# Kernel tuning notes

Hardware: AMD Instinct MI355X
Metric: run time of the kernel (lower is better)

The kernel has to match this reference:

```python
import jax, jax.numpy as jnp
import numpy as np
import math

DIM = 768
FFN_DIM = 4 * DIM
EPS = 1e-5

def layer_norm(x, gamma, beta):
    mu = jnp.mean(x, axis=-1, keepdims=True)
    var = jnp.var(x, axis=-1, keepdims=True)
    return (x - mu) * jax.lax.rsqrt(var + EPS) * gamma + beta

def setup_inputs() -> dict:
    key = jax.random.key(0)
    ks = jax.random.split(key, 8)
    b, n, d = 8, 2048, DIM
    s = 1.0 / math.sqrt(d)
    x = jax.random.normal(ks[0], (b, n, d), dtype=jnp.float32)
    Wq = jax.random.normal(ks[1], (d, d), dtype=jnp.float32) * s
    Wk = jax.random.normal(ks[2], (d, d), dtype=jnp.float32) * s
    Wv = jax.random.normal(ks[3], (d, d), dtype=jnp.float32) * s
    W1 = jax.random.normal(ks[4], (d, FFN_DIM), dtype=jnp.float32) * s
    b1 = jnp.zeros((FFN_DIM,), dtype=jnp.float32)
    W2 = jax.random.normal(ks[5], (FFN_DIM, d), dtype=jnp.float32) * (1.0 / math.sqrt(FFN_DIM))
    b2 = jnp.zeros((d,), dtype=jnp.float32)
    g1 = jnp.ones((d,), dtype=jnp.float32); be1 = jnp.zeros((d,), dtype=jnp.float32)
    g2 = jnp.ones((d,), dtype=jnp.float32); be2 = jnp.zeros((d,), dtype=jnp.float32)
    return {"x": x, "Wq": Wq, "Wk": Wk, "Wv": Wv, "ln1_g": g1, "ln1_b": be1,
            "W1": W1, "b1": b1, "W2": W2, "b2": b2, "ln2_g": g2, "ln2_b": be2}

def reference(x, Wq, Wk, Wv, ln1_g, ln1_b, W1, b1, W2, b2, ln2_g, ln2_b):
    # Self-attention (single head, full dim; dropout in eval mode => identity)
    Q = jnp.einsum('bnd,de->bne', x, Wq)
    K = jnp.einsum('bnd,de->bne', x, Wk)
    V = jnp.einsum('bnd,de->bne', x, Wv)
    scores = jnp.einsum('bnd,bmd->bnm', Q, K) / math.sqrt(DIM)  # [b,n,n]
    attn = jax.nn.softmax(scores, axis=-1)
    O = jnp.einsum('bnm,bmd->bnd', attn, V)
    h = layer_norm(x + O, ln1_g, ln1_b)
    # FFN with exact GELU (torch nn.GELU default)
    hidden = jax.nn.gelu(jnp.einsum('bnd,df->bnf', h, W1) + b1, approximate=False)
    out = jnp.einsum('bnf,fd->bnd', hidden, W2) + b2
    return layer_norm(h + out, ln2_g, ln2_b)
```

## Files before the change

### kernel.cpp

```cpp
#include <hip/hip_runtime.h>
#include <hip/hip_bf16.h>
#include <math.h>

using u16 = unsigned short;
typedef __bf16 bf16x8 __attribute__((ext_vector_type(8)));
typedef float f32x4 __attribute__((ext_vector_type(4)));
typedef u16 u16x8 __attribute__((ext_vector_type(8)));

__device__ __forceinline__ u16 f2b(float f) {
  union { float f; unsigned u; } c; c.f = f;
  unsigned r = c.u + 0x7fffu + ((c.u >> 16) & 1u);
  return (u16)(r >> 16);
}
__device__ __forceinline__ float b2f(u16 h) {
  union { unsigned u; float f; } c; c.u = ((unsigned)h) << 16;
  return c.f;
}

#define EPI_BF16 0
#define EPI_BF16_SCALE 1
#define EPI_GELU_BIAS 2
#define EPI_F32_BIAS 3

#define GLDS16(src, dst)                                                     \
  __builtin_amdgcn_global_load_lds(                                          \
      (const __attribute__((address_space(1))) void*)(src),                  \
      (__attribute__((address_space(3))) void*)(dst), 16, 0, 0)

__device__ __forceinline__ int xswz(int o, int n) {
  int q = n >> 3, r = n & 7, x = o & 7, i = o >> 3;
  return (x < r ? x * (q + 1) : r * (q + 1) + (x - r) * q) + i;
}

template <int EPI>
__global__ __launch_bounds__(512, 2) void gemm256(
    const u16* __restrict__ Ag, const u16* __restrict__ Bg,
    void* __restrict__ Cg, const float* __restrict__ bias,
    int nbx, int K, float scale, int lda, int ldb, int ldc,
    long long sAz, long long sBz, long long sCz)
{
  __shared__ __align__(16) u16 lds[65536];

  const int tid = threadIdx.x;
  const int wave = tid >> 6, lane = tid & 63;
  const int wr = wave >> 2, wc = wave & 3;
  const int id = xswz(blockIdx.x, gridDim.x);
  const int bx = id % nbx, by = id / nbx;
  const int m0 = by * 256, n0 = bx * 256;
  const long long z = blockIdx.z;
  const u16* A = Ag + z * sAz + (long long)m0 * lda;
  const u16* B = Bg + z * sBz + (long long)n0 * ldb;

  const int rA = wave * 32 + (lane >> 2);
  const int slot = (lane & 3) ^ ((rA >> 1) & 3);
  const u16* a0 = A + (long long)rA * lda + slot * 8;
  const u16* a1 = a0 + (long long)16 * lda;
  const u16* b0 = B + (long long)rA * ldb + slot * 8;
  const u16* b1 = b0 + (long long)16 * ldb;
  const int d0 = wave * 32 * 32;
  const int d1 = (wave * 32 + 16) * 32;

  int offA[8], offB[4];
#pragma unroll
  for (int mf = 0; mf < 8; ++mf) {
    int r = wr * 128 + mf * 16 + (lane & 15);
    int b = r * 64 + ((lane >> 4) << 4);
    offA[mf] = b ^ (((b >> 7) & 3) << 4);
  }
#pragma unroll
  for (int nf = 0; nf < 4; ++nf) {
    int r = wc * 64 + nf * 16 + (lane & 15);
    int b = r * 64 + ((lane >> 4) << 4);
    offB[nf] = b ^ (((b >> 7) & 3) << 4);
  }

  f32x4 acc[8][4];
#pragma unroll
  for (int m = 0; m < 8; ++m)
#pragma unroll
    for (int n = 0; n < 4; ++n) acc[m][n] = f32x4{0.f, 0.f, 0.f, 0.f};

  const char* ldsc = (const char*)lds;
  const int NT = K >> 6;

  GLDS16(a0, lds + 0 * 8192 + d0);  GLDS16(a1, lds + 0 * 8192 + d1);
  GLDS16(b0, lds + 2 * 8192 + d0);  GLDS16(b1, lds + 2 * 8192 + d1);
  GLDS16(a0 + 32, lds + 1 * 8192 + d0);  GLDS16(a1 + 32, lds + 1 * 8192 + d1);
  GLDS16(b0 + 32, lds + 3 * 8192 + d0);  GLDS16(b1 + 32, lds + 3 * 8192 + d1);
  asm volatile("s_waitcnt vmcnt(4)" ::: "memory");
  asm volatile("s_barrier" ::: "memory");

  for (int t = 0; t < NT; ++t) {
    const int buf = t & 1, nb = buf ^ 1;
    const int kc = (t + 1 < NT) ? ((t + 1) << 6) : 0;
    const char* pA0 = ldsc + (buf * 4 + 0) * 16384;
    const char* pA1 = ldsc + (buf * 4 + 1) * 16384;
    const char* pB0 = ldsc + (buf * 4 + 2) * 16384;
    const char* pB1 = ldsc + (buf * 4 + 3) * 16384;
    u16* q = lds + nb * 4 * 8192;

    bf16x8 Af[4], Bf[4];

    GLDS16(a0 + kc, q + 0 * 8192 + d0);
    GLDS16(a1 + kc, q + 0 * 8192 + d1);
#pragma unroll
    for (int m = 0; m < 4; ++m) Af[m] = *(const bf16x8*)(pA0 + offA[m]);
#pragma unroll
    for (int n = 0; n < 4; ++n) Bf[n] = *(const bf16x8*)(pB0 + offB[n]);
    asm volatile("s_barrier" ::: "memory");
    __builtin_amdgcn_s_setprio(1);
#pragma unroll
    for (int m = 0; m < 4; ++m)
#pragma unroll
      for (int n = 0; n < 4; ++n)
        acc[m][n] = __builtin_amdgcn_mfma_f32_16x16x32_bf16(Af[m], Bf[n], acc[m][n], 0, 0, 0);
    __builtin_amdgcn_s_setprio(0);
    asm volatile("s_barrier" ::: "memory");

    GLDS16(b0 + kc, q + 2 * 8192 + d0);
    GLDS16(b1 + kc, q + 2 * 8192 + d1);
#pragma unroll
    for (int m = 0; m < 4; ++m) Af[m] = *(const bf16x8*)(pA0 + offA[4 + m]);
    asm volatile("s_barrier" ::: "memory");
    __builtin_amdgcn_s_setprio(1);
#pragma unroll
    for (int m = 0; m < 4; ++m)
#pragma unroll
      for (int n = 0; n < 4; ++n)
        acc[4 + m][n] = __builtin_amdgcn_mfma_f32_16x16x32_bf16(Af[m], Bf[n], acc[4 + m][n], 0, 0, 0);
    __builtin_amdgcn_s_setprio(0);
    asm volatile("s_waitcnt vmcnt(4)" ::: "memory");
    asm volatile("s_barrier" ::: "memory");

    GLDS16(a0 + kc + 32, q + 1 * 8192 + d0);
    GLDS16(a1 + kc + 32, q + 1 * 8192 + d1);
#pragma unroll
    for (int m = 0; m < 4; ++m) Af[m] = *(const bf16x8*)(pA1 + offA[m]);
#pragma unroll
    for (int n = 0; n < 4; ++n) Bf[n] = *(const bf16x8*)(pB1 + offB[n]);
    asm volatile("s_barrier" ::: "memory");
    __builtin_amdgcn_s_setprio(1);
#pragma unroll
    for (int m = 0; m < 4; ++m)
#pragma unroll
      for (int n = 0; n < 4; ++n)
        acc[m][n] = __builtin_amdgcn_mfma_f32_16x16x32_bf16(Af[m], Bf[n], acc[m][n], 0, 0, 0);
    __builtin_amdgcn_s_setprio(0);
    asm volatile("s_barrier" ::: "memory");

    GLDS16(b0 + kc + 32, q + 3 * 8192 + d0);
    GLDS16(b1 + kc + 32, q + 3 * 8192 + d1);
#pragma unroll
    for (int m = 0; m < 4; ++m) Af[m] = *(const bf16x8*)(pA1 + offA[4 + m]);
    asm volatile("s_barrier" ::: "memory");
    __builtin_amdgcn_s_setprio(1);
#pragma unroll
    for (int m = 0; m < 4; ++m)
#pragma unroll
      for (int n = 0; n < 4; ++n)
        acc[4 + m][n] = __builtin_amdgcn_mfma_f32_16x16x32_bf16(Af[m], Bf[n], acc[4 + m][n], 0, 0, 0);
    __builtin_amdgcn_s_setprio(0);
    asm volatile("s_waitcnt vmcnt(4)" ::: "memory");
    asm volatile("s_barrier" ::: "memory");
  }

#pragma unroll
  for (int mf = 0; mf < 8; ++mf) {
#pragma unroll
    for (int nf = 0; nf < 4; ++nf) {
      const int crow = m0 + wr * 128 + mf * 16 + (lane >> 4) * 4;
      const int ccol = n0 + wc * 64 + nf * 16 + (lane & 15);
#pragma unroll
      for (int j = 0; j < 4; ++j) {
        const float v = acc[mf][nf][j];
        const long long off = (long long)(crow + j) * ldc + ccol + z * sCz;
        if (EPI == EPI_BF16) {
          ((u16*)Cg)[off] = f2b(v);
        } else if (EPI == EPI_BF16_SCALE) {
          ((u16*)Cg)[off] = f2b(v * scale);
        } else if (EPI == EPI_GELU_BIAS) {
          const float t2 = v + bias[ccol];
          const float g = 0.5f * t2 * (1.0f + erff(t2 * 0.70710678118654752440f));
          ((u16*)Cg)[off] = f2b(g);
        } else {
          ((float*)Cg)[off] = v + bias[ccol];
        }
      }
    }
  }
}

__global__ __launch_bounds__(256) void cast_f32_bf16(
    const float* __restrict__ x, u16* __restrict__ y, long long n4)
{
  const long long i = (long long)blockIdx.x * 256 + threadIdx.x;
  if (i >= n4) return;
  const float4 v = ((const float4*)x)[i];
  ushort4 o;
  o.x = f2b(v.x); o.y = f2b(v.y); o.z = f2b(v.z); o.w = f2b(v.w);
  ((ushort4*)y)[i] = o;
}

template <bool SRC_BF16>
__global__ __launch_bounds__(256) void transpose_cast(
    const void* __restrict__ srcv, u16* __restrict__ dst, int R, int C, int ldsrc,
    long long szSrc, long long szDst)
{
  __shared__ float tile[32][33];
  const long long zs = (long long)blockIdx.z * szSrc;
  const long long zd = (long long)blockIdx.z * szDst;
  const int c0 = blockIdx.x * 32, r0 = blockIdx.y * 32;
  const int tx = threadIdx.x & 31, ty = threadIdx.x >> 5;
#pragma unroll
  for (int i = 0; i < 4; ++i) {
    const int r = r0 + ty + i * 8;
    float v;
    if (SRC_BF16) v = b2f(((const u16*)srcv)[zs + (long long)r * ldsrc + c0 + tx]);
    else          v = ((const float*)srcv)[zs + (long long)r * ldsrc + c0 + tx];
    tile[ty + i * 8][tx] = v;
  }
  __syncthreads();
#pragma unroll
  for (int i = 0; i < 4; ++i) {
    const int c = c0 + ty + i * 8;
    dst[zd + (long long)c * R + r0 + tx] = f2b(tile[tx][ty + i * 8]);
  }
}

__global__ __launch_bounds__(256) void softmax_rows(
    u16* __restrict__ S, int ncol)
{
  __shared__ float red[8];
  const long long row = blockIdx.x;
  u16* s = S + row * ncol;
  const int t = threadIdx.x;

  const u16x8 u = *(const u16x8*)&s[t * 8];
  float v[8];
#pragma unroll
  for (int j = 0; j < 8; ++j) v[j] = b2f(u[j]);

  float mx = v[0];
#pragma unroll
  for (int j = 1; j < 8; ++j) mx = fmaxf(mx, v[j]);
  for (int o = 32; o; o >>= 1) mx = fmaxf(mx, __shfl_xor(mx, o));
  if ((t & 63) == 0) red[t >> 6] = mx;
  __syncthreads();
  mx = fmaxf(fmaxf(red[0], red[1]), fmaxf(red[2], red[3]));

  float sum = 0.f;
#pragma unroll
  for (int j = 0; j < 8; ++j) { v[j] = __expf(v[j] - mx); sum += v[j]; }
  for (int o = 32; o; o >>= 1) sum += __shfl_xor(sum, o);
  if ((t & 63) == 0) red[4 + (t >> 6)] = sum;
  __syncthreads();
  sum = red[4] + red[5] + red[6] + red[7];

  const float inv = 1.0f / sum;
  u16x8 o8;
#pragma unroll
  for (int j = 0; j < 8; ++j) o8[j] = f2b(v[j] * inv);
  *(u16x8*)&s[t * 8] = o8;
}

__global__ __launch_bounds__(256) void ln1_kernel(
    const float* __restrict__ x, const u16* __restrict__ O,
    const float* __restrict__ g, const float* __restrict__ be,
    u16* __restrict__ h)
{
  __shared__ float red[8];
  const long long row = blockIdx.x;
  const float* xr = x + row * 768;
  const u16* orow = O + row * 768;
  const int t = threadIdx.x, base = t * 3;

  float v[3];
#pragma unroll
  for (int j = 0; j < 3; ++j) v[j] = xr[base + j] + b2f(orow[base + j]);
  float s = v[0] + v[1] + v[2];
  float ss = v[0] * v[0] + v[1] * v[1] + v[2] * v[2];
  for (int o = 32; o; o >>= 1) { s += __shfl_xor(s, o); ss += __shfl_xor(ss, o); }
  if ((t & 63) == 0) { red[t >> 6] = s; red[4 + (t >> 6)] = ss; }
  __syncthreads();
  s = red[0] + red[1] + red[2] + red[3];
  ss = red[4] + red[5] + red[6] + red[7];
  const float mu = s * (1.0f / 768.0f);
  const float var = ss * (1.0f / 768.0f) - mu * mu;
  const float inv = rsqrtf(var + 1e-5f);
#pragma unroll
  for (int j = 0; j < 3; ++j) {
    const float o = (v[j] - mu) * inv * g[base + j] + be[base + j];
    h[row * 768 + base + j] = f2b(o);
  }
}

__global__ __launch_bounds__(256) void ln2_kernel(
    const u16* __restrict__ h, const float* __restrict__ oflt,
    const float* __restrict__ g, const float* __restrict__ be,
    float* __restrict__ y)
{
  __shared__ float red[8];
  const long long row = blockIdx.x;
  const u16* hr = h + row * 768;
  const float* orow = oflt + row * 768;
  const int t = threadIdx.x, base = t * 3;

  float v[3];
#pragma unroll
  for (int j = 0; j < 3; ++j) v[j] = b2f(hr[base + j]) + orow[base + j];
  float s = v[0] + v[1] + v[2];
  float ss = v[0] * v[0] + v[1] * v[1] + v[2] * v[2];
  for (int o = 32; o; o >>= 1) { s += __shfl_xor(s, o); ss += __shfl_xor(ss, o); }
  if ((t & 63) == 0) { red[t >> 6] = s; red[4 + (t >> 6)] = ss; }
  __syncthreads();
  s = red[0] + red[1] + red[2] + red[3];
  ss = red[4] + red[5] + red[6] + red[7];
  const float mu = s * (1.0f / 768.0f);
  const float var = ss * (1.0f / 768.0f) - mu * mu;
  const float inv = rsqrtf(var + 1e-5f);
#pragma unroll
  for (int j = 0; j < 3; ++j) {
    y[row * 768 + base + j] = (v[j] - mu) * inv * g[base + j] + be[base + j];
  }
}

extern "C" void kernel_launch(void* const* d_in, const int* in_sizes, int n_in,
                              void* d_out, int out_size, void* d_ws, size_t ws_size,
                              hipStream_t stream)
{
  const int Bb = 8, Nn = 2048, D = 768, F = 3072, E = 2304;
  const int M = Bb * Nn;
  const long long MD = (long long)M * D;

  const float* x   = (const float*)d_in[0];
  const float* Wq  = (const float*)d_in[1];
  const float* Wk  = (const float*)d_in[2];
  const float* Wv  = (const float*)d_in[3];
  const float* g1  = (const float*)d_in[4];
  const float* be1 = (const float*)d_in[5];
  const float* W1  = (const float*)d_in[6];
  const float* b1  = (const float*)d_in[7];
  const float* W2  = (const float*)d_in[8];
  const float* b2  = (const float*)d_in[9];
  const float* g2  = (const float*)d_in[10];
  const float* be2 = (const float*)d_in[11];

  u16* xb    = (u16*)d_out;
  u16* wqkvt = xb + MD;
  u16* wqt = wqkvt;
  u16* wkt = wqkvt + 768 * 768;
  u16* wvt = wqkvt + 2 * 768 * 768;

  char* w = (char*)d_ws;
  size_t off = 0;
  auto alloc = [&](size_t bytes) { void* p = w + off; off += bytes; return p; };
  u16* w1t = (u16*)alloc((size_t)F * D * 2);
  u16* w2t = (u16*)alloc((size_t)D * F * 2);
  u16* hb  = (u16*)alloc((size_t)MD * 2);
  u16* qkv = (u16*)alloc((size_t)M * E * 2);
  u16* Vt  = (u16*)alloc((size_t)Bb * D * Nn * 2);
  u16* S   = (u16*)alloc((size_t)Bb * Nn * Nn * 2);
  u16* O   = (u16*)alloc((size_t)MD * 2);
  u16*   hidden = qkv;
  float* outf   = (float*)S;

  const dim3 tcb(256);
  const float scl = 0.03608439182435161f;

  cast_f32_bf16<<<(unsigned)(MD / 4 / 256), 256, 0, stream>>>(x, xb, MD / 4);
  transpose_cast<false><<<dim3(D / 32, D / 32, 1), tcb, 0, stream>>>(Wq, wqt, D, D, D, 0, 0);
  transpose_cast<false><<<dim3(D / 32, D / 32, 1), tcb, 0, stream>>>(Wk, wkt, D, D, D, 0, 0);
  transpose_cast<false><<<dim3(D / 32, D / 32, 1), tcb, 0, stream>>>(Wv, wvt, D, D, D, 0, 0);
  transpose_cast<false><<<dim3(F / 32, D / 32, 1), tcb, 0, stream>>>(W1, w1t, D, F, F, 0, 0);
  transpose_cast<false><<<dim3(D / 32, F / 32, 1), tcb, 0, stream>>>(W2, w2t, F, D, D, 0, 0);

  gemm256<EPI_BF16><<<dim3(9 * 64, 1, 1), 512, 0, stream>>>(
      xb, wqkvt, qkv, nullptr, 9, D, 1.f, D, D, E, 0, 0, 0);

  transpose_cast<true><<<dim3(D / 32, Nn / 32, Bb), tcb, 0, stream>>>(
      qkv + 1536, Vt, Nn, D, E, (long long)Nn * E, (long long)D * Nn);

  gemm256<EPI_BF16_SCALE><<<dim3(8 * 8, 1, Bb), 512, 0, stream>>>(
      qkv, qkv + 768, S, nullptr, 8, D, scl, E, E, Nn,
      (long long)Nn * E, (long long)Nn * E, (long long)Nn * Nn);

  softmax_rows<<<M, 256, 0, stream>>>(S, Nn);

  gemm256<EPI_BF16><<<dim3(3 * 8, 1, Bb), 512, 0, stream>>>(
      S, Vt, O, nullptr, 3, Nn, 1.f, Nn, Nn, D,
      (long long)Nn * Nn, (long long)D * Nn, (long long)Nn * D);

  ln1_kernel<<<M, 256, 0, stream>>>(x, O, g1, be1, hb);

  gemm256<EPI_GELU_BIAS><<<dim3(12 * 64, 1, 1), 512, 0, stream>>>(
      hb, w1t, hidden, b1, 12, D, 1.f, D, D, F, 0, 0, 0);

  gemm256<EPI_F32_BIAS><<<dim3(3 * 64, 1, 1), 512, 0, stream>>>(
      hidden, w2t, outf, b2, 3, F, 1.f, F, F, D, 0, 0, 0);

  ln2_kernel<<<M, 256, 0, stream>>>(hb, outf, g2, be2, (float*)d_out);
}
```

Measured before the change: 529.2 us.

## Add 128x128 GEMM kernel for attention and FFN2; use fast tanh GELU

Introduces a 4-wave 128x128-tile GEMM variant and uses it for the QK^T, PV and FFN down-projection GEMMs, so that grids which previously underfilled the CUs launch more blocks. It also replaces the exact erf GELU epilogue with an exp-based tanh approximation to cut epilogue cost. Smaller tiles lower per-block data reuse, and the GELU approximation differs slightly from the exact form.

New measurement: 520.4 us. No clear change (-1.7%).

```diff
diff --git a/kernel.cpp b/kernel.cpp
--- a/kernel.cpp
+++ b/kernel.cpp
@@ -17,6 +17,12 @@
   return c.f;
 }
 
+__device__ __forceinline__ float fast_gelu(float t) {
+  float y = fminf(1.5957691216f * t + 0.07135481283f * t * t * t, 80.f);
+  float e = __expf(y);
+  return t * e * (1.0f / (e + 1.0f));
+}
+
 #define EPI_BF16 0
 #define EPI_BF16_SCALE 1
 #define EPI_GELU_BIAS 2
@@ -30,6 +36,21 @@
 __device__ __forceinline__ int xswz(int o, int n) {
   int q = n >> 3, r = n & 7, x = o & 7, i = o >> 3;
   return (x < r ? x * (q + 1) : r * (q + 1) + (x - r) * q) + i;
+}
+
+template <int EPI>
+__device__ __forceinline__ void epi_store(
+    void* Cg, const float* bias, float v, long long off, int ccol, float scale)
+{
+  if (EPI == EPI_BF16) {
+    ((u16*)Cg)[off] = f2b(v);
+  } else if (EPI == EPI_BF16_SCALE) {
+    ((u16*)Cg)[off] = f2b(v * scale);
+  } else if (EPI == EPI_GELU_BIAS) {
+    ((u16*)Cg)[off] = f2b(fast_gelu(v + bias[ccol]));
+  } else {
+    ((float*)Cg)[off] = v + bias[ccol];
+  }
 }
 
 template <int EPI>
@@ -172,19 +193,124 @@
       const int ccol = n0 + wc * 64 + nf * 16 + (lane & 15);
 #pragma unroll
       for (int j = 0; j < 4; ++j) {
-        const float v = acc[mf][nf][j];
         const long long off = (long long)(crow + j) * ldc + ccol + z * sCz;
-        if (EPI == EPI_BF16) {
-          ((u16*)Cg)[off] = f2b(v);
-        } else if (EPI == EPI_BF16_SCALE) {
-          ((u16*)Cg)[off] = f2b(v * scale);
-        } else if (EPI == EPI_GELU_BIAS) {
-          const float t2 = v + bias[ccol];
-          const float g = 0.5f * t2 * (1.0f + erff(t2 * 0.70710678118654752440f));
-          ((u16*)Cg)[off] = f2b(g);
-        } else {
-          ((float*)Cg)[off] = v + bias[ccol];
-        }
+        epi_store<EPI>(Cg, bias, acc[mf][nf][j], off, ccol, scale);
+      }
+    }
+  }
+}
+
+template <int EPI>
+__global__ __launch_bounds__(256, 2) void gemm128(
+    const u16* __restrict__ Ag, const u16* __restrict__ Bg,
+    void* __restrict__ Cg, const float* __restrict__ bias,
+    int nbx, int K, float scale, int lda, int ldb, int ldc,
+    long long sAz, long long sBz, long long sCz)
+{
+  __shared__ __align__(16) u16 lds[32768];
+
+  const int tid = threadIdx.x;
+  const int wave = tid >> 6, lane = tid & 63;
+  const int wr = wave >> 1, wc = wave & 1;
+  const int id = xswz(blockIdx.x, gridDim.x);
+  const int bx = id % nbx, by = id / nbx;
+  const int m0 = by * 128, n0 = bx * 128;
+  const long long z = blockIdx.z;
+  const u16* A = Ag + z * sAz + (long long)m0 * lda;
+  const u16* B = Bg + z * sBz + (long long)n0 * ldb;
+
+  const int rA = wave * 32 + (lane >> 2);
+  const int slot = (lane & 3) ^ ((rA >> 1) & 3);
+  const u16* a0 = A + (long long)rA * lda + slot * 8;
+  const u16* a1 = a0 + (long long)16 * lda;
+  const u16* b0 = B + (long long)rA * ldb + slot * 8;
+  const u16* b1 = b0 + (long long)16 * ldb;
+  const int d0 = wave * 32 * 32;
+  const int d1 = (wave * 32 + 16) * 32;
+
+  int offA[4], offB[4];
+#pragma unroll
+  for (int f = 0; f < 4; ++f) {
+    int ra = wr * 64 + f * 16 + (lane & 15);
+    int ba = ra * 64 + ((lane >> 4) << 4);
+    offA[f] = ba ^ (((ba >> 7) & 3) << 4);
+    int rb = wc * 64 + f * 16 + (lane & 15);
+    int bb = rb * 64 + ((lane >> 4) << 4);
+    offB[f] = bb ^ (((bb >> 7) & 3) << 4);
+  }
+
+  f32x4 acc[4][4];
+#pragma unroll
+  for (int m = 0; m < 4; ++m)
+#pragma unroll
+    for (int n = 0; n < 4; ++n) acc[m][n] = f32x4{0.f, 0.f, 0.f, 0.f};
+
+  const char* ldsc = (const char*)lds;
+  const int NT = K >> 6;
+
+  GLDS16(a0, lds + 0 * 4096 + d0);  GLDS16(a1, lds + 0 * 4096 + d1);
+  GLDS16(b0, lds + 2 * 4096 + d0);  GLDS16(b1, lds + 2 * 4096 + d1);
+  GLDS16(a0 + 32, lds + 1 * 4096 + d0);  GLDS16(a1 + 32, lds + 1 * 4096 + d1);
+  GLDS16(b0 + 32, lds + 3 * 4096 + d0);  GLDS16(b1 + 32, lds + 3 * 4096 + d1);
+  asm volatile("s_waitcnt vmcnt(4)" ::: "memory");
+  asm volatile("s_barrier" ::: "memory");
+
+  for (int t = 0; t < NT; ++t) {
+    const int buf = t & 1, nb = buf ^ 1;
+    const int kc = (t + 1 < NT) ? ((t + 1) << 6) : 0;
+    const char* pA0 = ldsc + (buf * 4 + 0) * 8192;
+    const char* pA1 = ldsc + (buf * 4 + 1) * 8192;
+    const char* pB0 = ldsc + (buf * 4 + 2) * 8192;
+    const char* pB1 = ldsc + (buf * 4 + 3) * 8192;
+    u16* q = lds + nb * 4 * 4096;
+
+    bf16x8 Af[4], Bf[4];
+
+    GLDS16(a0 + kc, q + 0 * 4096 + d0);  GLDS16(a1 + kc, q + 0 * 4096 + d1);
+    GLDS16(b0 + kc, q + 2 * 4096 + d0);  GLDS16(b1 + kc, q + 2 * 4096 + d1);
+#pragma unroll
+    for (int m = 0; m < 4; ++m) Af[m] = *(const bf16x8*)(pA0 + offA[m]);
+#pragma unroll
+    for (int n = 0; n < 4; ++n) Bf[n] = *(const bf16x8*)(pB0 + offB[n]);
+    asm volatile("s_barrier" ::: "memory");
+    __builtin_amdgcn_s_setprio(1);
+#pragma unroll
+    for (int m = 0; m < 4; ++m)
+#pragma unroll
+      for (int n = 0; n < 4; ++n)
+        acc[m][n] = __builtin_amdgcn_mfma_f32_16x16x32_bf16(Af[m], Bf[n], acc[m][n], 0, 0, 0);
+    __builtin_amdgcn_s_setprio(0);
+    asm volatile("s_waitcnt vmcnt(4)" ::: "memory");
+    asm volatile("s_barrier" ::: "memory");
+
+    GLDS16(a0 + kc + 32, q + 1 * 4096 + d0);  GLDS16(a1 + kc + 32, q + 1 * 4096 + d1);
+    GLDS16(b0 + kc + 32, q + 3 * 4096 + d0);  GLDS16(b1 + kc + 32, q + 3 * 4096 + d1);
+#pragma unroll
+    for (int m = 0; m < 4; ++m) Af[m] = *(const bf16x8*)(pA1 + offA[m]);
+#pragma unroll
+    for (int n = 0; n < 4; ++n) Bf[n] = *(const bf16x8*)(pB1 + offB[n]);
+    asm volatile("s_barrier" ::: "memory");
+    __builtin_amdgcn_s_setprio(1);
+#pragma unroll
+    for (int m = 0; m < 4; ++m)
+#pragma unroll
+      for (int n = 0; n < 4; ++n)
+        acc[m][n] = __builtin_amdgcn_mfma_f32_16x16x32_bf16(Af[m], Bf[n], acc[m][n], 0, 0, 0);
+    __builtin_amdgcn_s_setprio(0);
+    asm volatile("s_waitcnt vmcnt(4)" ::: "memory");
+    asm volatile("s_barrier" ::: "memory");
+  }
+
+#pragma unroll
+  for (int mf = 0; mf < 4; ++mf) {
+#pragma unroll
+    for (int nf = 0; nf < 4; ++nf) {
+      const int crow = m0 + wr * 64 + mf * 16 + (lane >> 4) * 4;
+      const int ccol = n0 + wc * 64 + nf * 16 + (lane & 15);
+#pragma unroll
+      for (int j = 0; j < 4; ++j) {
+        const long long off = (long long)(crow + j) * ldc + ccol + z * sCz;
+        epi_store<EPI>(Cg, bias, acc[mf][nf][j], off, ccol, scale);
       }
     }
   }
@@ -380,14 +506,14 @@
   transpose_cast<true><<<dim3(D / 32, Nn / 32, Bb), tcb, 0, stream>>>(
       qkv + 1536, Vt, Nn, D, E, (long long)Nn * E, (long long)D * Nn);
 
-  gemm256<EPI_BF16_SCALE><<<dim3(8 * 8, 1, Bb), 512, 0, stream>>>(
-      qkv, qkv + 768, S, nullptr, 8, D, scl, E, E, Nn,
+  gemm128<EPI_BF16_SCALE><<<dim3(16 * 16, 1, Bb), 256, 0, stream>>>(
+      qkv, qkv + 768, S, nullptr, 16, D, scl, E, E, Nn,
       (long long)Nn * E, (long long)Nn * E, (long long)Nn * Nn);
 
   softmax_rows<<<M, 256, 0, stream>>>(S, Nn);
 
-  gemm256<EPI_BF16><<<dim3(3 * 8, 1, Bb), 512, 0, stream>>>(
-      S, Vt, O, nullptr, 3, Nn, 1.f, Nn, Nn, D,
+  gemm128<EPI_BF16><<<dim3(6 * 16, 1, Bb), 256, 0, stream>>>(
+      S, Vt, O, nullptr, 6, Nn, 1.f, Nn, Nn, D,
       (long long)Nn * Nn, (long long)D * Nn, (long long)Nn * D);
 
   ln1_kernel<<<M, 256, 0, stream>>>(x, O, g1, be1, hb);
@@ -395,8 +521,8 @@
   gemm256<EPI_GELU_BIAS><<<dim3(12 * 64, 1, 1), 512, 0, stream>>>(
       hb, w1t, hidden, b1, 12, D, 1.f, D, D, F, 0, 0, 0);
 
-  gemm256<EPI_F32_BIAS><<<dim3(3 * 64, 1, 1), 512, 0, stream>>>(
-      hidden, w2t, outf, b2, 3, F, 1.f, F, F, D, 0, 0, 0);
+  gemm128<EPI_F32_BIAS><<<dim3(6 * 128, 1, 1), 256, 0, stream>>>(
+      hidden, w2t, outf, b2, 6, F, 1.f, F, F, D, 0, 0, 0);
 
   ln2_kernel<<<M, 256, 0, stream>>>(hb, outf, g2, be2, (float*)d_out);
 }
```

## Replace 256x256 double-buffered GEMM with 128x128 four-stage ring pipeline and tanh-form GELU

Applied to the files above, without the earlier changes.

Swaps the 256x256-tile, 8-wave double-buffered GEMM for a 128x128-tile, 4-wave kernel that streams K in 32-wide slices through a four-slot LDS ring, keeping three slices in flight with one barrier per slice. Smaller tiles give four times as many blocks, so the CUs fill better on the small GEMMs. The cost is less operand reuse per block and more global traffic. The exact erf GELU is also replaced by a sigmoid/tanh approximation using __expf, which is cheaper but less accurate.

Result: slower. 548.8 us (+3.7%).

```diff
diff --git a/kernel.cpp b/kernel.cpp
--- a/kernel.cpp
+++ b/kernel.cpp
@@ -17,6 +17,12 @@
   return c.f;
 }
 
+__device__ __forceinline__ float fast_gelu(float t) {
+  float y = fminf(1.5957691216f * t + 0.07135481283f * t * t * t, 80.f);
+  float e = __expf(y);
+  return t * e * (1.0f / (e + 1.0f));
+}
+
 #define EPI_BF16 0
 #define EPI_BF16_SCALE 1
 #define EPI_GELU_BIAS 2
@@ -33,81 +39,95 @@
 }
 
 template <int EPI>
-__global__ __launch_bounds__(512, 2) void gemm256(
+__device__ __forceinline__ void epi_store(
+    void* Cg, const float* bias, float v, long long off, int ccol, float scale)
+{
+  if (EPI == EPI_BF16) {
+    ((u16*)Cg)[off] = f2b(v);
+  } else if (EPI == EPI_BF16_SCALE) {
+    ((u16*)Cg)[off] = f2b(v * scale);
+  } else if (EPI == EPI_GELU_BIAS) {
+    ((u16*)Cg)[off] = f2b(fast_gelu(v + bias[ccol]));
+  } else {
+    ((float*)Cg)[off] = v + bias[ccol];
+  }
+}
+
+template <int EPI>
+__global__ __launch_bounds__(256, 2) void gemm_ring(
     const u16* __restrict__ Ag, const u16* __restrict__ Bg,
     void* __restrict__ Cg, const float* __restrict__ bias,
     int nbx, int K, float scale, int lda, int ldb, int ldc,
     long long sAz, long long sBz, long long sCz)
 {
-  __shared__ __align__(16) u16 lds[65536];
+  __shared__ __align__(16) u16 lds[32768];
 
   const int tid = threadIdx.x;
   const int wave = tid >> 6, lane = tid & 63;
-  const int wr = wave >> 2, wc = wave & 3;
+  const int wr = wave >> 1, wc = wave & 1;
   const int id = xswz(blockIdx.x, gridDim.x);
   const int bx = id % nbx, by = id / nbx;
-  const int m0 = by * 256, n0 = bx * 256;
+  const int m0 = by * 128, n0 = bx * 128;
   const long long z = blockIdx.z;
   const u16* A = Ag + z * sAz + (long long)m0 * lda;
   const u16* B = Bg + z * sBz + (long long)n0 * ldb;
 
   const int rA = wave * 32 + (lane >> 2);
-  const int slot = (lane & 3) ^ ((rA >> 1) & 3);
-  const u16* a0 = A + (long long)rA * lda + slot * 8;
+  const int slot4 = (lane & 3) ^ ((rA >> 1) & 3);
+  const u16* a0 = A + (long long)rA * lda + slot4 * 8;
   const u16* a1 = a0 + (long long)16 * lda;
-  const u16* b0 = B + (long long)rA * ldb + slot * 8;
+  const u16* b0 = B + (long long)rA * ldb + slot4 * 8;
   const u16* b1 = b0 + (long long)16 * ldb;
-  const int d0 = wave * 32 * 32;
-  const int d1 = (wave * 32 + 16) * 32;
-
-  int offA[8], offB[4];
-#pragma unroll
-  for (int mf = 0; mf < 8; ++mf) {
-    int r = wr * 128 + mf * 16 + (lane & 15);
-    int b = r * 64 + ((lane >> 4) << 4);
-    offA[mf] = b ^ (((b >> 7) & 3) << 4);
-  }
-#pragma unroll
-  for (int nf = 0; nf < 4; ++nf) {
-    int r = wc * 64 + nf * 16 + (lane & 15);
-    int b = r * 64 + ((lane >> 4) << 4);
-    offB[nf] = b ^ (((b >> 7) & 3) << 4);
-  }
-
-  f32x4 acc[8][4];
-#pragma unroll
-  for (int m = 0; m < 8; ++m)
+  const int dw = wave * 1024;
+
+  int offA[4], offB[4];
+#pragma unroll
+  for (int f = 0; f < 4; ++f) {
+    int ra = wr * 64 + f * 16 + (lane & 15);
+    int ba = ra * 64 + ((lane >> 4) << 4);
+    offA[f] = ba ^ (((ba >> 7) & 3) << 4);
+    int rb = wc * 64 + f * 16 + (lane & 15);
+    int bb = rb * 64 + ((lane >> 4) << 4);
+    offB[f] = bb ^ (((bb >> 7) & 3) << 4);
+  }
+
+  f32x4 acc[4][4];
+#pragma unroll
+  for (int m = 0; m < 4; ++m)
 #pragma unroll
     for (int n = 0; n < 4; ++n) acc[m][n] = f32x4{0.f, 0.f, 0.f, 0.f};
 
   const char* ldsc = (const char*)lds;
-  const int NT = K >> 6;
-
-  GLDS16(a0, lds + 0 * 8192 + d0);  GLDS16(a1, lds + 0 * 8192 + d1);
-  GLDS16(b0, lds + 2 * 8192 + d0);  GLDS16(b1, lds + 2 * 8192 + d1);
-  GLDS16(a0 + 32, lds + 1 * 8192 + d0);  GLDS16(a1 + 32, lds + 1 * 8192 + d1);
-  GLDS16(b0 + 32, lds + 3 * 8192 + d0);  GLDS16(b1 + 32, lds + 3 * 8192 + d1);
-  asm volatile("s_waitcnt vmcnt(4)" ::: "memory");
+  const int NH = K >> 5;
+
+#pragma unroll
+  for (int s = 0; s < 3; ++s) {
+    const int kc = s * 32;
+    GLDS16(a0 + kc, lds + s * 8192 + dw);
+    GLDS16(a1 + kc, lds + s * 8192 + dw + 512);
+    GLDS16(b0 + kc, lds + s * 8192 + 4096 + dw);
+    GLDS16(b1 + kc, lds + s * 8192 + 4096 + dw + 512);
+  }
+  asm volatile("s_waitcnt vmcnt(8)" ::: "memory");
   asm volatile("s_barrier" ::: "memory");
 
-  for (int t = 0; t < NT; ++t) {
-    const int buf = t & 1, nb = buf ^ 1;
-    const int kc = (t + 1 < NT) ? ((t + 1) << 6) : 0;
-    const char* pA0 = ldsc + (buf * 4 + 0) * 16384;
-    const char* pA1 = ldsc + (buf * 4 + 1) * 16384;
-    const char* pB0 = ldsc + (buf * 4 + 2) * 16384;
-    const char* pB1 = ldsc + (buf * 4 + 3) * 16384;
-    u16* q = lds + nb * 4 * 8192;
-
+#pragma unroll 4
+  for (int h = 0; h < NH; ++h) {
+    const int hp = (h + 3 < NH) ? h + 3 : h + 3 - NH;
+    const int sw = (h + 3) & 3;
+    const int kc = hp << 5;
+    GLDS16(a0 + kc, lds + sw * 8192 + dw);
+    GLDS16(a1 + kc, lds + sw * 8192 + dw + 512);
+    GLDS16(b0 + kc, lds + sw * 8192 + 4096 + dw);
+    GLDS16(b1 + kc, lds + sw * 8192 + 4096 + dw + 512);
+
+    const char* pA = ldsc + (h & 3) * 16384;
+    const char* pB = pA + 8192;
     bf16x8 Af[4], Bf[4];
-
-    GLDS16(a0 + kc, q + 0 * 8192 + d0);
-    GLDS16(a1 + kc, q + 0 * 8192 + d1);
-#pragma unroll
-    for (int m = 0; m < 4; ++m) Af[m] = *(const bf16x8*)(pA0 + offA[m]);
-#pragma unroll
-    for (int n = 0; n < 4; ++n) Bf[n] = *(const bf16x8*)(pB0 + offB[n]);
-    asm volatile("s_barrier" ::: "memory");
+#pragma unroll
+    for (int m = 0; m < 4; ++m) Af[m] = *(const bf16x8*)(pA + offA[m]);
+#pragma unroll
+    for (int n = 0; n < 4; ++n) Bf[n] = *(const bf16x8*)(pB + offB[n]);
     __builtin_amdgcn_s_setprio(1);
 #pragma unroll
     for (int m = 0; m < 4; ++m)
@@ -115,76 +135,20 @@
       for (int n = 0; n < 4; ++n)
         acc[m][n] = __builtin_amdgcn_mfma_f32_16x16x32_bf16(Af[m], Bf[n], acc[m][n], 0, 0, 0);
     __builtin_amdgcn_s_setprio(0);
+    asm volatile("s_waitcnt vmcnt(8)" ::: "memory");
     asm volatile("s_barrier" ::: "memory");
-
-    GLDS16(b0 + kc, q + 2 * 8192 + d0);
-    GLDS16(b1 + kc, q + 2 * 8192 + d1);
-#pragma unroll
-    for (int m = 0; m < 4; ++m) Af[m] = *(const bf16x8*)(pA0 + offA[4 + m]);
-    asm volatile("s_barrier" ::: "memory");
-    __builtin_amdgcn_s_setprio(1);
-#pragma unroll
-    for (int m = 0; m < 4; ++m)
-#pragma unroll
-      for (int n = 0; n < 4; ++n)
-        acc[4 + m][n] = __builtin_amdgcn_mfma_f32_16x16x32_bf16(Af[m], Bf[n], acc[4 + m][n], 0, 0, 0);
-    __builtin_amdgcn_s_setprio(0);
-    asm volatile("s_waitcnt vmcnt(4)" ::: "memory");
-    asm volatile("s_barrier" ::: "memory");
-
-    GLDS16(a0 + kc + 32, q + 1 * 8192 + d0);
-    GLDS16(a1 + kc + 32, q + 1 * 8192 + d1);
-#pragma unroll
-    for (int m = 0; m < 4; ++m) Af[m] = *(const bf16x8*)(pA1 + offA[m]);
-#pragma unroll
-    for (int n = 0; n < 4; ++n) Bf[n] = *(const bf16x8*)(pB1 + offB[n]);
-    asm volatile("s_barrier" ::: "memory");
-    __builtin_amdgcn_s_setprio(1);
-#pragma unroll
-    for (int m = 0; m < 4; ++m)
-#pragma unroll
-      for (int n = 0; n < 4; ++n)
-        acc[m][n] = __builtin_amdgcn_mfma_f32_16x16x32_bf16(Af[m], Bf[n], acc[m][n], 0, 0, 0);
-    __builtin_amdgcn_s_setprio(0);
-    asm volatile("s_barrier" ::: "memory");
-
-    GLDS16(b0 + kc + 32, q + 3 * 8192 + d0);
-    GLDS16(b1 + kc + 32, q + 3 * 8192 + d1);
-#pragma unroll
-    for (int m = 0; m < 4; ++m) Af[m] = *(const bf16x8*)(pA1 + offA[4 + m]);
-    asm volatile("s_barrier" ::: "memory");
-    __builtin_amdgcn_s_setprio(1);
-#pragma unroll
-    for (int m = 0; m < 4; ++m)
-#pragma unroll
-      for (int n = 0; n < 4; ++n)
-        acc[4 + m][n] = __builtin_amdgcn_mfma_f32_16x16x32_bf16(Af[m], Bf[n], acc[4 + m][n], 0, 0, 0);
-    __builtin_amdgcn_s_setprio(0);
-    asm volatile("s_waitcnt vmcnt(4)" ::: "memory");
-    asm volatile("s_barrier" ::: "memory");
-  }
-
-#pragma unroll
-  for (int mf = 0; mf < 8; ++mf) {
+  }
+
+#pragma unroll
+  for (int mf = 0; mf < 4; ++mf) {
 #pragma unroll
     for (int nf = 0; nf < 4; ++nf) {
-      const int crow = m0 + wr * 128 + mf * 16 + (lane >> 4) * 4;
+      const int crow = m0 + wr * 64 + mf * 16 + (lane >> 4) * 4;
       const int ccol = n0 + wc * 64 + nf * 16 + (lane & 15);
 #pragma unroll
       for (int j = 0; j < 4; ++j) {
-        const float v = acc[mf][nf][j];
         const long long off = (long long)(crow + j) * ldc + ccol + z * sCz;
-        if (EPI == EPI_BF16) {
-          ((u16*)Cg)[off] = f2b(v);
-        } else if (EPI == EPI_BF16_SCALE) {
-          ((u16*)Cg)[off] = f2b(v * scale);
-        } else if (EPI == EPI_GELU_BIAS) {
-          const float t2 = v + bias[ccol];
-          const float g = 0.5f * t2 * (1.0f + erff(t2 * 0.70710678118654752440f));
-          ((u16*)Cg)[off] = f2b(g);
-        } else {
-          ((float*)Cg)[off] = v + bias[ccol];
-        }
+        epi_store<EPI>(Cg, bias, acc[mf][nf][j], off, ccol, scale);
       }
     }
   }
@@ -374,29 +338,29 @@
   transpose_cast<false><<<dim3(F / 32, D / 32, 1), tcb, 0, stream>>>(W1, w1t, D, F, F, 0, 0);
   transpose_cast<false><<<dim3(D / 32, F / 32, 1), tcb, 0, stream>>>(W2, w2t, F, D, D, 0, 0);
 
-  gemm256<EPI_BF16><<<dim3(9 * 64, 1, 1), 512, 0, stream>>>(
-      xb, wqkvt, qkv, nullptr, 9, D, 1.f, D, D, E, 0, 0, 0);
+  gemm_ring<EPI_BF16><<<dim3(18 * 128, 1, 1), 256, 0, stream>>>(
+      xb, wqkvt, qkv, nullptr, 18, D, 1.f, D, D, E, 0, 0, 0);
 
   transpose_cast<true><<<dim3(D / 32, Nn / 32, Bb), tcb, 0, stream>>>(
       qkv + 1536, Vt, Nn, D, E, (long long)Nn * E, (long long)D * Nn);
 
-  gemm256<EPI_BF16_SCALE><<<dim3(8 * 8, 1, Bb), 512, 0, stream>>>(
-      qkv, qkv + 768, S, nullptr, 8, D, scl, E, E, Nn,
+  gemm_ring<EPI_BF16_SCALE><<<dim3(16 * 16, 1, Bb), 256, 0, stream>>>(
+      qkv, qkv + 768, S, nullptr, 16, D, scl, E, E, Nn,
       (long long)Nn * E, (long long)Nn * E, (long long)Nn * Nn);
 
   softmax_rows<<<M, 256, 0, stream>>>(S, Nn);
 
-  gemm256<EPI_BF16><<<dim3(3 * 8, 1, Bb), 512, 0, stream>>>(
-      S, Vt, O, nullptr, 3, Nn, 1.f, Nn, Nn, D,
+  gemm_ring<EPI_BF16><<<dim3(6 * 16, 1, Bb), 256, 0, stream>>>(
+      S, Vt, O, nullptr, 6, Nn, 1.f, Nn, Nn, D,
       (long long)Nn * Nn, (long long)D * Nn, (long long)Nn * D);
 
   ln1_kernel<<<M, 256, 0, stream>>>(x, O, g1, be1, hb);
 
-  gemm256<EPI_GELU_BIAS><<<dim3(12 * 64, 1, 1), 512, 0, stream>>>(
-      hb, w1t, hidden, b1, 12, D, 1.f, D, D, F, 0, 0, 0);
-
-  gemm256<EPI_F32_BIAS><<<dim3(3 * 64, 1, 1), 512, 0, stream>>>(
-      hidden, w2t, outf, b2, 3, F, 1.f, F, F, D, 0, 0, 0);
+  gemm_ring<EPI_GELU_BIAS><<<dim3(24 * 128, 1, 1), 256, 0, stream>>>(
+      hb, w1t, hidden, b1, 24, D, 1.f, D, D, F, 0, 0, 0);
+
+  gemm_ring<EPI_F32_BIAS><<<dim3(6 * 128, 1, 1), 256, 0, stream>>>(
+      hidden, w2t, outf, b2, 6, F, 1.f, F, F, D, 0, 0, 0);
 
   ln2_kernel<<<M, 256, 0, stream>>>(hb, outf, g2, be2, (float*)d_out);
 }
```
